# Optimization experiments

Measured on AMD Instinct MI355X. Metric: run time of the kernel, lower is better.

Reference implementation:

```python
import jax, jax.numpy as jnp
import numpy as np

B, S, D, H = 2, 2048, 1024, 16
DEPTH = D // H

def setup_inputs() -> dict:
    key = jax.random.key(0)
    k1, k2, k3 = jax.random.split(key, 3)
    x = jax.random.normal(k1, (B, S, D), dtype=jnp.float32)
    # causal mask (1 = attend, 0 = blocked), broadcastable over batch/heads
    mask = jnp.tril(jnp.ones((S, S), dtype=jnp.int32))[None, None]
    W_qkv = jax.random.normal(k2, (D, 3 * D), dtype=jnp.float32) * (D ** -0.5)
    b_qkv = jnp.zeros((3 * D,), dtype=jnp.float32)
    W_out = jax.random.normal(k3, (D, D), dtype=jnp.float32) * (D ** -0.5)
    b_out = jnp.zeros((D,), dtype=jnp.float32)
    return {"x": x, "mask": mask, "W_qkv": W_qkv, "b_qkv": b_qkv,
            "W_out": W_out, "b_out": b_out}

def reference(x, mask, W_qkv, b_qkv, W_out, b_out):
    b, s, _ = x.shape
    qkv = x @ W_qkv + b_qkv                        # [b, s, 3D]
    qkv = qkv.reshape(b, s, H, 3 * DEPTH)          # matches torch reshape
    qkv = jnp.transpose(qkv, (0, 2, 1, 3))         # [b, h, s, 3*depth]
    q, k, v = jnp.split(qkv, 3, axis=-1)           # each [b, h, s, depth]
    scores = jnp.einsum('bhqd,bhkd->bhqk', q, k) / jnp.sqrt(jnp.float32(DEPTH))
    scores = jnp.where(mask == 0, -jnp.inf, scores)
    attn = jax.nn.softmax(scores, axis=-1)         # dropout: eval mode (identity)
    out = jnp.einsum('bhqk,bhkd->bhqd', attn, v)   # [b, h, s, depth]
    out = jnp.transpose(out, (0, 2, 1, 3)).reshape(b, s, D)
    return out @ W_out + b_out
```

## Files before the change

### kernel.cpp

```cpp
#include <hip/hip_runtime.h>

#define BB 2
#define SS 2048
#define DDIM 1024
#define HH 16
#define DEPTH 64
#define QKVN (3*DDIM)

typedef unsigned short u16;
typedef unsigned int u32;
typedef __attribute__((ext_vector_type(8))) short bf16x8;
typedef __attribute__((ext_vector_type(4))) float f32x4;

__device__ __forceinline__ u16 f2bf(float f){
  union{float f; u32 u;} z; z.f=f;
  u32 r = z.u + 0x7fffu + ((z.u>>16)&1u);
  return (u16)(r>>16);
}
#define NEG_BIG (-1e30f)

#define GL2LDS(gp, lp) __builtin_amdgcn_global_load_lds( \
    (const __attribute__((address_space(1))) void*)(gp), \
    (__attribute__((address_space(3))) void*)(lp), 16, 0, 0)

__global__ void convT_k(const float* __restrict__ in, u16* __restrict__ out, int R, int C){
  __shared__ float tile[32][33];
  int c0 = blockIdx.x<<5, r0 = blockIdx.y<<5;
  int tx = threadIdx.x, ty = threadIdx.y;
  for (int i=ty;i<32;i+=8) tile[i][tx] = in[(size_t)(r0+i)*C + c0+tx];
  __syncthreads();
  for (int i=ty;i<32;i+=8) out[(size_t)(c0+i)*R + r0+tx] = f2bf(tile[tx][i]);
}

__global__ void convX_k(const float* __restrict__ in, u16* __restrict__ out){
  size_t i = ((size_t)blockIdx.x*256 + threadIdx.x) * 8;
  float4 a = *(const float4*)(in + i);
  float4 b = *(const float4*)(in + i + 4);
  ushort4 lo = { f2bf(a.x), f2bf(a.y), f2bf(a.z), f2bf(a.w) };
  ushort4 hi = { f2bf(b.x), f2bf(b.y), f2bf(b.z), f2bf(b.w) };
  *(ushort4*)(out + i)     = lo;
  *(ushort4*)(out + i + 4) = hi;
}

__global__ __launch_bounds__(256,2) void gemm_qkv_k(
    const u16* __restrict__ A, const u16* __restrict__ Bt,
    const float* __restrict__ bias,
    u16* __restrict__ Qb, u16* __restrict__ Kb, u16* __restrict__ Vt)
{
  const int K = DDIM;
  __shared__ __align__(16) u16 As[128*32];
  __shared__ __align__(16) u16 Bs[128*32];
  const int tid = threadIdx.x;
  const int m0 = blockIdx.x<<7, n0 = blockIdx.y<<7;
  const int w = tid>>6, lane = tid&63, q = lane>>4, ln = lane&15;
  const int wr = (w>>1)<<6, wc = (w&1)<<6;

  f32x4 acc[4][4];
  #pragma unroll
  for (int i=0;i<4;i++)
    #pragma unroll
    for (int j=0;j<4;j++) acc[i][j] = (f32x4){0.f,0.f,0.f,0.f};

  const int row0 = tid>>2,         off0 = (tid&3)<<3;
  const int row1 = (tid+256)>>2,   off1 = (tid&3)<<3;

  for (int k0=0;k0<K;k0+=32){
    GL2LDS(&A [(size_t)(m0+row0)*K + k0 + off0], &As[(row0<<5)+off0]);
    GL2LDS(&Bt[(size_t)(n0+row0)*K + k0 + off0], &Bs[(row0<<5)+off0]);
    GL2LDS(&A [(size_t)(m0+row1)*K + k0 + off1], &As[(row1<<5)+off1]);
    GL2LDS(&Bt[(size_t)(n0+row1)*K + k0 + off1], &Bs[(row1<<5)+off1]);
    __syncthreads();
    bf16x8 af[4], bfr[4];
    #pragma unroll
    for (int i=0;i<4;i++) af[i]  = *(const bf16x8*)&As[((wr + (i<<4) + ln)<<5) + (q<<3)];
    #pragma unroll
    for (int j=0;j<4;j++) bfr[j] = *(const bf16x8*)&Bs[((wc + (j<<4) + ln)<<5) + (q<<3)];
    #pragma unroll
    for (int i=0;i<4;i++)
      #pragma unroll
      for (int j=0;j<4;j++)
        acc[i][j] = __builtin_amdgcn_mfma_f32_16x16x32_bf16(af[i], bfr[j], acc[i][j], 0, 0, 0);
    __syncthreads();
  }

  #pragma unroll
  for (int i=0;i<4;i++){
    const int mmb = m0 + wr + (i<<4) + (q<<2);
    const int bsel = mmb >> 11;
    const int sb   = mmb & 2047;
    #pragma unroll
    for (int j=0;j<4;j++){
      const int n = n0 + wc + (j<<4) + ln;
      const int h = n / 192;
      const int rr = n - h*192;
      const int bh = (bsel<<4) + h;
      const float bv = bias[n];
      if (rr < 64){
        u16* dst = Qb + (size_t)bh*SS*DEPTH + rr;
        #pragma unroll
        for (int r=0;r<4;r++) dst[(size_t)(sb+r)*DEPTH] = f2bf((acc[i][j][r] + bv)*0.125f);
      } else if (rr < 128){
        u16* dst = Kb + (size_t)bh*SS*DEPTH + (rr-64);
        #pragma unroll
        for (int r=0;r<4;r++) dst[(size_t)(sb+r)*DEPTH] = f2bf(acc[i][j][r] + bv);
      } else {
        ushort4 pv = { f2bf(acc[i][j][0] + bv), f2bf(acc[i][j][1] + bv),
                       f2bf(acc[i][j][2] + bv), f2bf(acc[i][j][3] + bv) };
        *(ushort4*)(Vt + ((size_t)bh*DEPTH + (rr-128))*SS + sb) = pv;
      }
    }
  }
}

__global__ __launch_bounds__(256,4) void attn_k(
    u16* __restrict__ Qb, const u16* __restrict__ Kb, const u16* __restrict__ Vt)
{
  __shared__ __align__(16) u16 Ks[64*72];
  __shared__ __align__(16) u16 VsT[64*72];
  __shared__ __align__(16) u16 ps[4][16*72];

  const int tid = threadIdx.x, w = tid>>6, lane = tid&63, q = lane>>4, ln = lane&15;
  const int bh = blockIdx.x;
  const int y  = blockIdx.y, sgrp = y>>3, rr_ = y&7;
  const int qt = (sgrp==0) ? 31-rr_ : (sgrp==1) ? 16+rr_ : (sgrp==2) ? 15-rr_ : rr_;
  const int r0 = qt<<6;
  const size_t kbase = (size_t)bh*SS*DEPTH;
  const size_t vbase = (size_t)bh*DEPTH*SS;
  const u16* __restrict__ Kp = Kb + kbase;
  const u16* __restrict__ Vp = Vt + vbase;

  const int j0 = tid>>3,      d0 = (tid&7)<<3;
  const int j1 = j0 + 32,     d1 = d0;

  bf16x8 qf[2];
  #pragma unroll
  for (int ks=0;ks<2;ks++)
    qf[ks] = *(const bf16x8*)(Qb + kbase + (size_t)(r0 + (w<<4) + ln)*DEPTH + (ks<<5) + (q<<3));

  const bf16x8 vone = { (short)0x3F80, (short)0x3F80, (short)0x3F80, (short)0x3F80,
                        (short)0x3F80, (short)0x3F80, (short)0x3F80, (short)0x3F80 };

  f32x4 o[4];
  #pragma unroll
  for (int nt=0;nt<4;nt++) o[nt] = (f32x4){0.f,0.f,0.f,0.f};
  f32x4 lacc = (f32x4){0.f,0.f,0.f,0.f};
  float m_r[4];
  #pragma unroll
  for (int r=0;r<4;r++) m_r[r] = NEG_BIG;

  uint4 kr0, kr1, vr0, vr1;
  #define LOADT(t) do { \
    kr0 = *(const uint4*)(Kp + (size_t)(((t)<<6)+j0)*DEPTH + d0); \
    kr1 = *(const uint4*)(Kp + (size_t)(((t)<<6)+j1)*DEPTH + d1); \
    vr0 = *(const uint4*)(Vp + (size_t)j0*SS + ((t)<<6) + d0); \
    vr1 = *(const uint4*)(Vp + (size_t)j1*SS + ((t)<<6) + d1); } while(0)

  const int T = qt + 1;
  LOADT(0);
  for (int t=0;t<T;t++){
    if (t) __syncthreads();
    *(uint4*)&Ks [j0*72 + d0] = kr0;
    *(uint4*)&Ks [j1*72 + d1] = kr1;
    *(uint4*)&VsT[j0*72 + d0] = vr0;
    *(uint4*)&VsT[j1*72 + d1] = vr1;
    if (t+1 < T) LOADT(t+1);
    __syncthreads();

    f32x4 sc[4];
    #pragma unroll
    for (int jt=0;jt<4;jt++) sc[jt] = (f32x4){0.f,0.f,0.f,0.f};
    #pragma unroll
    for (int ks=0;ks<2;ks++){
      #pragma unroll
      for (int jt=0;jt<4;jt++){
        bf16x8 kf = *(const bf16x8*)&Ks[((jt<<4)+ln)*72 + (ks<<5) + (q<<3)];
        sc[jt] = __builtin_amdgcn_mfma_f32_16x16x32_bf16(qf[ks], kf, sc[jt], 0, 0, 0);
      }
    }

    if (t == T-1){
      const int rowb = r0 + (w<<4) + (q<<2);
      #pragma unroll
      for (int jt=0;jt<4;jt++){
        const int col = (t<<6) + (jt<<4) + ln;
        #pragma unroll
        for (int r=0;r<4;r++)
          if (col > rowb + r) sc[jt][r] = NEG_BIG;
      }
    }

    float alpha_r[4];
    #pragma unroll
    for (int r=0;r<4;r++){
      float mt = fmaxf(fmaxf(sc[0][r], sc[1][r]), fmaxf(sc[2][r], sc[3][r]));
      #pragma unroll
      for (int off=1; off<16; off<<=1) mt = fmaxf(mt, __shfl_xor(mt, off));
      const float mnew = fmaxf(m_r[r], mt);
      alpha_r[r] = __expf(m_r[r] - mnew);
      float p0 = __expf(sc[0][r]-mnew), p1 = __expf(sc[1][r]-mnew);
      float p2 = __expf(sc[2][r]-mnew), p3 = __expf(sc[3][r]-mnew);
      const int mrow = (q<<2) + r;
      ps[w][mrow*72 +      ln] = f2bf(p0);
      ps[w][mrow*72 + 16 + ln] = f2bf(p1);
      ps[w][mrow*72 + 32 + ln] = f2bf(p2);
      ps[w][mrow*72 + 48 + ln] = f2bf(p3);
      m_r[r] = mnew;
    }
    #pragma unroll
    for (int r=0;r<4;r++){
      lacc[r] *= alpha_r[r];
      #pragma unroll
      for (int nt=0;nt<4;nt++) o[nt][r] *= alpha_r[r];
    }

    #pragma unroll
    for (int ks=0;ks<2;ks++){
      bf16x8 pa = *(const bf16x8*)&ps[w][ln*72 + (ks<<5) + (q<<3)];
      lacc = __builtin_amdgcn_mfma_f32_16x16x32_bf16(pa, vone, lacc, 0, 0, 0);
      #pragma unroll
      for (int nt=0;nt<4;nt++){
        bf16x8 vf = *(const bf16x8*)&VsT[((nt<<4)+ln)*72 + (ks<<5) + (q<<3)];
        o[nt] = __builtin_amdgcn_mfma_f32_16x16x32_bf16(pa, vf, o[nt], 0, 0, 0);
      }
    }
  }
  #undef LOADT

  #pragma unroll
  for (int r=0;r<4;r++){
    const float rl = 1.f / fmaxf(lacc[r], 1e-30f);
    const int s = r0 + (w<<4) + (q<<2) + r;
    #pragma unroll
    for (int nt=0;nt<4;nt++)
      Qb[kbase + (size_t)s*DEPTH + (nt<<4) + ln] = f2bf(o[nt][r] * rl);
  }
}

__global__ __launch_bounds__(256,2) void gemm_out_k(
    const u16* __restrict__ Aq, const u16* __restrict__ Bt,
    const float* __restrict__ bias, float* __restrict__ out)
{
  const int K = DDIM;
  __shared__ __align__(16) u16 As[64*32];
  __shared__ __align__(16) u16 Bs[128*32];
  const int tid = threadIdx.x;
  const int m0 = blockIdx.x<<6, n0 = blockIdx.y<<7;
  const int bsel = m0>>11, ms = m0&2047;
  const int w = tid>>6, lane = tid&63, q = lane>>4, ln = lane&15;
  const int wr = (w>>1)<<5, wc = (w&1)<<6;

  f32x4 acc[2][4];
  #pragma unroll
  for (int i=0;i<2;i++)
    #pragma unroll
    for (int j=0;j<4;j++) acc[i][j] = (f32x4){0.f,0.f,0.f,0.f};

  const int rowA  = tid>>2,       offA = (tid&3)<<3;
  const int rowB0 = tid>>2,       offB = (tid&3)<<3;
  const int rowB1 = (tid+256)>>2;

  for (int k0=0;k0<K;k0+=32){
    const size_t abase = (size_t)((bsel<<4) + (k0>>6))*SS*DEPTH + (k0&63);
    GL2LDS(&Aq[abase + (size_t)(ms+rowA)*DEPTH + offA], &As[(rowA<<5)+offA]);
    GL2LDS(&Bt[(size_t)(n0+rowB0)*K + k0 + offB],       &Bs[(rowB0<<5)+offB]);
    GL2LDS(&Bt[(size_t)(n0+rowB1)*K + k0 + offB],       &Bs[(rowB1<<5)+offB]);
    __syncthreads();
    bf16x8 af[2], bfr[4];
    #pragma unroll
    for (int i=0;i<2;i++) af[i]  = *(const bf16x8*)&As[((wr + (i<<4) + ln)<<5) + (q<<3)];
    #pragma unroll
    for (int j=0;j<4;j++) bfr[j] = *(const bf16x8*)&Bs[((wc + (j<<4) + ln)<<5) + (q<<3)];
    #pragma unroll
    for (int i=0;i<2;i++)
      #pragma unroll
      for (int j=0;j<4;j++)
        acc[i][j] = __builtin_amdgcn_mfma_f32_16x16x32_bf16(af[i], bfr[j], acc[i][j], 0, 0, 0);
    __syncthreads();
  }

  #pragma unroll
  for (int i=0;i<2;i++){
    #pragma unroll
    for (int j=0;j<4;j++){
      const int n = n0 + wc + (j<<4) + ln;
      const float bv = bias[n];
      #pragma unroll
      for (int r=0;r<4;r++){
        const int mm = m0 + wr + (i<<4) + (q<<2) + r;
        out[(size_t)mm*DDIM + n] = acc[i][j][r] + bv;
      }
    }
  }
}

extern "C" void kernel_launch(void* const* d_in, const int* in_sizes, int n_in,
                              void* d_out, int out_size, void* d_ws, size_t ws_size,
                              hipStream_t stream)
{
  int ix = 0, iw = 2, ibq = 3, iwo = 4, ibo = 5;
  if (n_in == 5){ iw = 1; ibq = 2; iwo = 3; ibo = 4; }
  const float* x  = (const float*)d_in[ix];
  const float* Wq = (const float*)d_in[iw];
  const float* bq = (const float*)d_in[ibq];
  const float* Wo = (const float*)d_in[iwo];
  const float* bo = (const float*)d_in[ibo];
  float* out = (float*)d_out;

  u16* ws  = (u16*)d_ws;
  u16* Wqt = ws;
  u16* Wot = Wqt + (size_t)QKVN*DDIM;
  u16* Qb  = Wot + (size_t)DDIM*DDIM;
  u16* Kb  = Qb  + (size_t)BB*HH*SS*DEPTH;
  u16* Vt  = Kb  + (size_t)BB*HH*SS*DEPTH;
  u16* xb  = Vt  + (size_t)BB*HH*SS*DEPTH;

  convT_k<<<dim3(QKVN/32, DDIM/32), dim3(32,8), 0, stream>>>(Wq, Wqt, DDIM, QKVN);
  convT_k<<<dim3(DDIM/32, DDIM/32), dim3(32,8), 0, stream>>>(Wo, Wot, DDIM, DDIM);
  convX_k<<<dim3(BB*SS*DDIM/2048), 256, 0, stream>>>(x, xb);

  gemm_qkv_k<<<dim3(BB*SS/128, QKVN/128), 256, 0, stream>>>(xb, Wqt, bq, Qb, Kb, Vt);
  attn_k    <<<dim3(BB*HH, 32),           256, 0, stream>>>(Qb, Kb, Vt);
  gemm_out_k<<<dim3(BB*SS/64,  DDIM/128), 256, 0, stream>>>(Qb, Wot, bo, out);
}
```

Measured before the change: 202.7 us.

## Process 128 query rows per attention block to reuse K/V tiles

Each attention block now handles two 64-row query sub-tiles (128 rows) instead of one, so every K/V tile staged in shared memory feeds twice as many MFMAs. The causal diagonal is handled by skipping the first sub-tile on the last key tile, with a separate mask per sub-tile, and the grid drops from 32 to 16 blocks per head. This halves global K/V traffic and barrier count per query row, but doubles accumulator registers and the P staging buffer, and leaves 512 blocks of coarser, more unbalanced work.

Result: slower. 274.5 us (+35.4%).

```diff
diff --git a/kernel.cpp b/kernel.cpp
--- a/kernel.cpp
+++ b/kernel.cpp
@@ -117,13 +117,13 @@
 {
   __shared__ __align__(16) u16 Ks[64*72];
   __shared__ __align__(16) u16 VsT[64*72];
-  __shared__ __align__(16) u16 ps[4][16*72];
+  __shared__ __align__(16) u16 ps[4][32*72];
 
   const int tid = threadIdx.x, w = tid>>6, lane = tid&63, q = lane>>4, ln = lane&15;
   const int bh = blockIdx.x;
-  const int y  = blockIdx.y, sgrp = y>>3, rr_ = y&7;
-  const int qt = (sgrp==0) ? 31-rr_ : (sgrp==1) ? 16+rr_ : (sgrp==2) ? 15-rr_ : rr_;
-  const int r0 = qt<<6;
+  const int y  = blockIdx.y;
+  const int qt = (y<8) ? 15-y : y-8;
+  const int r0 = qt<<7;
   const size_t kbase = (size_t)bh*SS*DEPTH;
   const size_t vbase = (size_t)bh*DEPTH*SS;
   const u16* __restrict__ Kp = Kb + kbase;
@@ -132,21 +132,29 @@
   const int j0 = tid>>3,      d0 = (tid&7)<<3;
   const int j1 = j0 + 32,     d1 = d0;
 
-  bf16x8 qf[2];
-  #pragma unroll
-  for (int ks=0;ks<2;ks++)
-    qf[ks] = *(const bf16x8*)(Qb + kbase + (size_t)(r0 + (w<<4) + ln)*DEPTH + (ks<<5) + (q<<3));
+  bf16x8 qf[2][2];
+  #pragma unroll
+  for (int rt=0;rt<2;rt++)
+    #pragma unroll
+    for (int ks=0;ks<2;ks++)
+      qf[rt][ks] = *(const bf16x8*)(Qb + kbase +
+          (size_t)(r0 + (rt<<6) + (w<<4) + ln)*DEPTH + (ks<<5) + (q<<3));
 
   const bf16x8 vone = { (short)0x3F80, (short)0x3F80, (short)0x3F80, (short)0x3F80,
                         (short)0x3F80, (short)0x3F80, (short)0x3F80, (short)0x3F80 };
 
-  f32x4 o[4];
-  #pragma unroll
-  for (int nt=0;nt<4;nt++) o[nt] = (f32x4){0.f,0.f,0.f,0.f};
-  f32x4 lacc = (f32x4){0.f,0.f,0.f,0.f};
-  float m_r[4];
-  #pragma unroll
-  for (int r=0;r<4;r++) m_r[r] = NEG_BIG;
+  f32x4 o[2][4];
+  #pragma unroll
+  for (int rt=0;rt<2;rt++)
+    #pragma unroll
+    for (int nt=0;nt<4;nt++) o[rt][nt] = (f32x4){0.f,0.f,0.f,0.f};
+  f32x4 lacc[2];
+  lacc[0] = (f32x4){0.f,0.f,0.f,0.f}; lacc[1] = (f32x4){0.f,0.f,0.f,0.f};
+  float m_r[2][4];
+  #pragma unroll
+  for (int rt=0;rt<2;rt++)
+    #pragma unroll
+    for (int r=0;r<4;r++) m_r[rt][r] = NEG_BIG;
 
   uint4 kr0, kr1, vr0, vr1;
   #define LOADT(t) do { \
@@ -155,7 +163,7 @@
     vr0 = *(const uint4*)(Vp + (size_t)j0*SS + ((t)<<6) + d0); \
     vr1 = *(const uint4*)(Vp + (size_t)j1*SS + ((t)<<6) + d1); } while(0)
 
-  const int T = qt + 1;
+  const int T = (qt<<1) + 2;
   LOADT(0);
   for (int t=0;t<T;t++){
     if (t) __syncthreads();
@@ -166,73 +174,89 @@
     if (t+1 < T) LOADT(t+1);
     __syncthreads();
 
-    f32x4 sc[4];
-    #pragma unroll
-    for (int jt=0;jt<4;jt++) sc[jt] = (f32x4){0.f,0.f,0.f,0.f};
+    #pragma unroll
+    for (int rt=0;rt<2;rt++){
+      if (rt==0 && t==T-1) continue;
+
+      f32x4 sc[4];
+      #pragma unroll
+      for (int jt=0;jt<4;jt++) sc[jt] = (f32x4){0.f,0.f,0.f,0.f};
+      #pragma unroll
+      for (int ks=0;ks<2;ks++){
+        #pragma unroll
+        for (int jt=0;jt<4;jt++){
+          bf16x8 kf = *(const bf16x8*)&Ks[((jt<<4)+ln)*72 + (ks<<5) + (q<<3)];
+          sc[jt] = __builtin_amdgcn_mfma_f32_16x16x32_bf16(qf[rt][ks], kf, sc[jt], 0, 0, 0);
+        }
+      }
+
+      if (t == T-2+rt){
+        const int rowb = r0 + (rt<<6) + (w<<4) + (q<<2);
+        #pragma unroll
+        for (int jt=0;jt<4;jt++){
+          const int col = (t<<6) + (jt<<4) + ln;
+          #pragma unroll
+          for (int r=0;r<4;r++)
+            if (col > rowb + r) sc[jt][r] = NEG_BIG;
+        }
+      }
+
+      float alpha_r[4];
+      #pragma unroll
+      for (int r=0;r<4;r++){
+        float mt = fmaxf(fmaxf(sc[0][r], sc[1][r]), fmaxf(sc[2][r], sc[3][r]));
+        #pragma unroll
+        for (int off=1; off<16; off<<=1) mt = fmaxf(mt, __shfl_xor(mt, off));
+        const float mnew = fmaxf(m_r[rt][r], mt);
+        alpha_r[r] = __expf(m_r[rt][r] - mnew);
+        float p0 = __expf(sc[0][r]-mnew), p1 = __expf(sc[1][r]-mnew);
+        float p2 = __expf(sc[2][r]-mnew), p3 = __expf(sc[3][r]-mnew);
+        const int mrow = (rt<<4) + (q<<2) + r;
+        ps[w][mrow*72 +      ln] = f2bf(p0);
+        ps[w][mrow*72 + 16 + ln] = f2bf(p1);
+        ps[w][mrow*72 + 32 + ln] = f2bf(p2);
+        ps[w][mrow*72 + 48 + ln] = f2bf(p3);
+        m_r[rt][r] = mnew;
+      }
+      #pragma unroll
+      for (int r=0;r<4;r++){
+        lacc[rt][r] *= alpha_r[r];
+        #pragma unroll
+        for (int nt=0;nt<4;nt++) o[rt][nt][r] *= alpha_r[r];
+      }
+    }
+
+    const bool rt0a = (t < T-1);
     #pragma unroll
     for (int ks=0;ks<2;ks++){
-      #pragma unroll
-      for (int jt=0;jt<4;jt++){
-        bf16x8 kf = *(const bf16x8*)&Ks[((jt<<4)+ln)*72 + (ks<<5) + (q<<3)];
-        sc[jt] = __builtin_amdgcn_mfma_f32_16x16x32_bf16(qf[ks], kf, sc[jt], 0, 0, 0);
-      }
-    }
-
-    if (t == T-1){
-      const int rowb = r0 + (w<<4) + (q<<2);
-      #pragma unroll
-      for (int jt=0;jt<4;jt++){
-        const int col = (t<<6) + (jt<<4) + ln;
-        #pragma unroll
-        for (int r=0;r<4;r++)
-          if (col > rowb + r) sc[jt][r] = NEG_BIG;
-      }
-    }
-
-    float alpha_r[4];
-    #pragma unroll
-    for (int r=0;r<4;r++){
-      float mt = fmaxf(fmaxf(sc[0][r], sc[1][r]), fmaxf(sc[2][r], sc[3][r]));
-      #pragma unroll
-      for (int off=1; off<16; off<<=1) mt = fmaxf(mt, __shfl_xor(mt, off));
-      const float mnew = fmaxf(m_r[r], mt);
-      alpha_r[r] = __expf(m_r[r] - mnew);
-      float p0 = __expf(sc[0][r]-mnew), p1 = __expf(sc[1][r]-mnew);
-      float p2 = __expf(sc[2][r]-mnew), p3 = __expf(sc[3][r]-mnew);
-      const int mrow = (q<<2) + r;
-      ps[w][mrow*72 +      ln] = f2bf(p0);
-      ps[w][mrow*72 + 16 + ln] = f2bf(p1);
-      ps[w][mrow*72 + 32 + ln] = f2bf(p2);
-      ps[w][mrow*72 + 48 + ln] = f2bf(p3);
-      m_r[r] = mnew;
-    }
-    #pragma unroll
-    for (int r=0;r<4;r++){
-      lacc[r] *= alpha_r[r];
-      #pragma unroll
-      for (int nt=0;nt<4;nt++) o[nt][r] *= alpha_r[r];
-    }
-
-    #pragma unroll
-    for (int ks=0;ks<2;ks++){
-      bf16x8 pa = *(const bf16x8*)&ps[w][ln*72 + (ks<<5) + (q<<3)];
-      lacc = __builtin_amdgcn_mfma_f32_16x16x32_bf16(pa, vone, lacc, 0, 0, 0);
+      bf16x8 pa1 = *(const bf16x8*)&ps[w][(16+ln)*72 + (ks<<5) + (q<<3)];
+      bf16x8 pa0;
+      lacc[1] = __builtin_amdgcn_mfma_f32_16x16x32_bf16(pa1, vone, lacc[1], 0, 0, 0);
+      if (rt0a){
+        pa0 = *(const bf16x8*)&ps[w][ln*72 + (ks<<5) + (q<<3)];
+        lacc[0] = __builtin_amdgcn_mfma_f32_16x16x32_bf16(pa0, vone, lacc[0], 0, 0, 0);
+      }
       #pragma unroll
       for (int nt=0;nt<4;nt++){
         bf16x8 vf = *(const bf16x8*)&VsT[((nt<<4)+ln)*72 + (ks<<5) + (q<<3)];
-        o[nt] = __builtin_amdgcn_mfma_f32_16x16x32_bf16(pa, vf, o[nt], 0, 0, 0);
+        o[1][nt] = __builtin_amdgcn_mfma_f32_16x16x32_bf16(pa1, vf, o[1][nt], 0, 0, 0);
+        if (rt0a)
+          o[0][nt] = __builtin_amdgcn_mfma_f32_16x16x32_bf16(pa0, vf, o[0][nt], 0, 0, 0);
       }
     }
   }
   #undef LOADT
 
   #pragma unroll
-  for (int r=0;r<4;r++){
-    const float rl = 1.f / fmaxf(lacc[r], 1e-30f);
-    const int s = r0 + (w<<4) + (q<<2) + r;
-    #pragma unroll
-    for (int nt=0;nt<4;nt++)
-      Qb[kbase + (size_t)s*DEPTH + (nt<<4) + ln] = f2bf(o[nt][r] * rl);
+  for (int rt=0;rt<2;rt++){
+    #pragma unroll
+    for (int r=0;r<4;r++){
+      const float rl = 1.f / fmaxf(lacc[rt][r], 1e-30f);
+      const int s = r0 + (rt<<6) + (w<<4) + (q<<2) + r;
+      #pragma unroll
+      for (int nt=0;nt<4;nt++)
+        Qb[kbase + (size_t)s*DEPTH + (nt<<4) + ln] = f2bf(o[rt][nt][r] * rl);
+    }
   }
 }
 
@@ -319,6 +343,6 @@
   convX_k<<<dim3(BB*SS*DDIM/2048), 256, 0, stream>>>(x, xb);
 
   gemm_qkv_k<<<dim3(BB*SS/128, QKVN/128), 256, 0, stream>>>(xb, Wqt, bq, Qb, Kb, Vt);
-  attn_k    <<<dim3(BB*HH, 32),           256, 0, stream>>>(Qb, Kb, Vt);
+  attn_k    <<<dim3(BB*HH, 16),           256, 0, stream>>>(Qb, Kb, Vt);
   gemm_out_k<<<dim3(BB*SS/64,  DDIM/128), 256, 0, stream>>>(Qb, Wot, bo, out);
 }
```
